# Performance work log

Measured on AMD Instinct MI355X. Metric: run time of the kernel, lower is better.

The kernel has to match this reference:

```python
import jax, jax.numpy as jnp
import numpy as np

PS = 14            # patch size
EMBED = 1024       # vision embed dim
LLM = 2048         # llm embed dim
DS = 2             # downsample factor
B = 8
GRID = 64          # H = W = 64 patches per image
MAX_POS = 4096
ROPE_THETA = 10000.0


def _rope_cache(dim, max_pos, base):
    inv_freq = 1.0 / (base ** (jnp.arange(0, dim, 2, dtype=jnp.float32) / dim))
    t = jnp.arange(max_pos, dtype=jnp.float32)
    freqs = jnp.outer(t, inv_freq)  # [max_pos, dim//2]
    return jnp.cos(freqs), jnp.sin(freqs)


def setup_inputs() -> dict:
    key = jax.random.key(0)
    ks = jax.random.split(key, 5)
    n_total = B * GRID * GRID
    pixel_values = jax.random.normal(ks[0], (n_total, 3, PS, PS), jnp.float32)
    patch_w = jax.random.normal(ks[1], (EMBED, 3, PS, PS), jnp.float32) * (1.0 / np.sqrt(3 * PS * PS))
    patch_b = jax.random.normal(ks[2], (EMBED,), jnp.float32) * 0.02
    dense_w = jax.random.normal(ks[3], (LLM, EMBED, DS, DS), jnp.float32) * (1.0 / np.sqrt(EMBED * DS * DS))
    dense_b = jax.random.normal(ks[4], (LLM,), jnp.float32) * 0.02
    rope_dim = EMBED // 2
    cos_x, sin_x = _rope_cache(rope_dim, MAX_POS, ROPE_THETA)
    cos_y, sin_y = _rope_cache(rope_dim, MAX_POS, ROPE_THETA)
    grid_hw = jnp.full((B, 2), GRID, dtype=jnp.int32)
    return {"pixel_values": pixel_values, "grid_hw": grid_hw,
            "patch_w": patch_w, "patch_b": patch_b,
            "dense_w": dense_w, "dense_b": dense_b,
            "cos_x": cos_x, "sin_x": sin_x, "cos_y": cos_y, "sin_y": sin_y}


def _apply_rotary_1d(x, cos_c, sin_c, pos):
    # x: [N, d], cos_c/sin_c: [max_pos, d//2], pos: [N] int
    c = cos_c[pos]  # gather: [N, d//2]
    s = sin_c[pos]
    x1 = x[:, 0::2]
    x2 = x[:, 1::2]
    o1 = x1 * c - x2 * s
    o2 = x1 * s + x2 * c
    return jnp.stack([o1, o2], axis=-1).reshape(x.shape)  # re-interleave


def _positions(grid_np):
    # grid metadata is static host-side data; build per-patch (x, y) coords
    xs, ys = [], []
    for h, w in grid_np:
        pid = np.arange(h * w)
        xs.append(pid % w)
        ys.append(pid // w)
    return jnp.asarray(np.concatenate(xs)), jnp.asarray(np.concatenate(ys))


def reference(pixel_values, grid_hw, patch_w, patch_b, dense_w, dense_b,
              cos_x, sin_x, cos_y, sin_y):
    grid_np = np.asarray(grid_hw)
    # patchify conv (kernel == stride == patch) is a per-patch linear proj
    pe = jnp.einsum('nchw,echw->ne', pixel_values, patch_w) + patch_b  # [N, E]
    pe = jax.nn.gelu(pe, approximate=False)
    abs_x, abs_y = _positions(grid_np)
    half = EMBED // 2
    p1 = _apply_rotary_1d(pe[:, :half], cos_x, sin_x, abs_x)
    p2 = _apply_rotary_1d(pe[:, half:], cos_y, sin_y, abs_y)
    pe = jnp.concatenate([p1, p2], axis=-1)  # [N, E]
    # per-image downsample conv (kernel == stride == DS): 2x2 block linear
    outs = []
    cur = 0
    for h, w in grid_np:
        x = pe[cur:cur + h * w].reshape(h // DS, DS, w // DS, DS, EMBED)
        o = jnp.einsum('hpwqe,oepq->hwo', x, dense_w) + dense_b
        outs.append(o.reshape(-1, LLM))
        cur += h * w
    return jnp.concatenate(outs, axis=0)
```

## Files before the change

kernel.cpp:

```cpp
#include <hip/hip_runtime.h>
#include <cstdint>


using f16x8 = __attribute__((ext_vector_type(8))) _Float16;
using f32x4 = __attribute__((ext_vector_type(4))) float;

__device__ __forceinline__ void gload_lds16(const void* g, void* l) {
  __builtin_amdgcn_global_load_lds(
      reinterpret_cast<const __attribute__((address_space(1))) unsigned int*>(
          reinterpret_cast<uintptr_t>(g)),
      reinterpret_cast<__attribute__((address_space(3))) unsigned int*>(
          reinterpret_cast<uintptr_t>(l)),
      16, 0, 0);
}

#define BAR   asm volatile("s_barrier" ::: "memory")
#define LGKM0 asm volatile("s_waitcnt lgkmcnt(0)" ::: "memory")
#define VM0   asm volatile("s_waitcnt vmcnt(0)" ::: "memory")

#define KP 640


__global__ void conv_w_kernel(const float* __restrict__ w1,
                              const float* __restrict__ w2,
                              const float* __restrict__ pix,
                              _Float16* __restrict__ h1,
                              _Float16* __restrict__ h2,
                              _Float16* __restrict__ pf) {
  const int bid = blockIdx.x;
  if (bid < 2560) {
    int i = bid * 256 + threadIdx.x;
    int e = i / KP;
    int k = i - e * KP;
    float v = (k < 588) ? w1[(size_t)e * 588 + k] : 0.0f;
    h1[i] = (_Float16)v;
  } else if (bid < 2560 + 8192) {
    int j = (bid - 2560) * 256 + threadIdx.x;
    int o = j >> 10;
    int e = j & 1023;
    const float4 v = *(const float4*)(w2 + (size_t)o * 4096 + e * 4);
    h2[(size_t)o * 4096 + e]        = (_Float16)v.x;
    h2[(size_t)o * 4096 + 1024 + e] = (_Float16)v.y;
    h2[(size_t)o * 4096 + 2048 + e] = (_Float16)v.z;
    h2[(size_t)o * 4096 + 3072 + e] = (_Float16)v.w;
  } else {
    int j = (bid - 2560 - 8192) * 256 + threadIdx.x;
    int n = j / (KP / 8);
    int g = j - n * (KP / 8);
    int k0 = g * 8;
    f16x8 v;
    if (k0 + 8 <= 588) {
      const float4 x0 = *(const float4*)(pix + (size_t)n * 588 + k0);
      const float4 x1 = *(const float4*)(pix + (size_t)n * 588 + k0 + 4);
      v[0] = (_Float16)x0.x; v[1] = (_Float16)x0.y;
      v[2] = (_Float16)x0.z; v[3] = (_Float16)x0.w;
      v[4] = (_Float16)x1.x; v[5] = (_Float16)x1.y;
      v[6] = (_Float16)x1.z; v[7] = (_Float16)x1.w;
    } else {
#pragma unroll
      for (int t = 0; t < 8; ++t) {
        int k = k0 + t;
        v[t] = (k < 588) ? (_Float16)pix[(size_t)n * 588 + k] : (_Float16)0.0f;
      }
    }
    *(f16x8*)(pf + (size_t)n * KP + k0) = v;
  }
}


#define MFMA16(I0, J0, AV, BV)                                                \
  _Pragma("unroll") for (int i_ = 0; i_ < 4; ++i_)                            \
  _Pragma("unroll") for (int j_ = 0; j_ < 2; ++j_)                            \
  _Pragma("unroll") for (int k_ = 0; k_ < 2; ++k_)                            \
      acc[(I0) + i_][(J0) + j_] = __builtin_amdgcn_mfma_f32_16x16x32_f16(     \
          AV[i_][k_], BV[j_][k_], acc[(I0) + i_][(J0) + j_], 0, 0, 0);

#define TILE_BODY(sb)                                                         \
  {                                                                           \
    f16x8 a0[4][2], a1[4][2], vb0[2][2], vb1[2][2];                           \
    _Pragma("unroll") for (int i = 0; i < 4; ++i) {                           \
      a0[i][0] = *(const f16x8*)(lbase + (sb) + aoff + i * 2048 + so0);       \
      a0[i][1] = *(const f16x8*)(lbase + (sb) + aoff + i * 2048 + so1);       \
    }                                                                         \
    _Pragma("unroll") for (int j = 0; j < 2; ++j) {                           \
      vb0[j][0] = *(const f16x8*)(lbase + (sb) + boff + j * 2048 + so0);      \
      vb0[j][1] = *(const f16x8*)(lbase + (sb) + boff + j * 2048 + so1);      \
    }                                                                         \
    MFMA16(0, 0, a0, vb0);                                                    \
    _Pragma("unroll") for (int j = 0; j < 2; ++j) {                           \
      vb1[j][0] = *(const f16x8*)(lbase + (sb) + boff + (2+j) * 2048 + so0);  \
      vb1[j][1] = *(const f16x8*)(lbase + (sb) + boff + (2+j) * 2048 + so1);  \
    }                                                                         \
    MFMA16(0, 2, a0, vb1);                                                    \
    _Pragma("unroll") for (int i = 0; i < 4; ++i) {                           \
      a1[i][0] = *(const f16x8*)(lbase + (sb) + aoff + (4+i) * 2048 + so0);   \
      a1[i][1] = *(const f16x8*)(lbase + (sb) + aoff + (4+i) * 2048 + so1);   \
    }                                                                         \
    MFMA16(4, 2, a1, vb1);                                                    \
    MFMA16(4, 0, a1, vb0);                                                    \
  }


__global__ __launch_bounds__(512, 2) void patch_gemm15(
    const _Float16* __restrict__ pixf,
    const _Float16* __restrict__ b1w,
    const float* __restrict__ bias1,
    const float* __restrict__ cosx, const float* __restrict__ sinx,
    const float* __restrict__ cosy, const float* __restrict__ siny,
    _Float16* __restrict__ peM)
{
  __shared__ _Float16 lds[2][256][64];

  const int tid  = threadIdx.x;
  const int lane = tid & 63;
  const int wave = tid >> 6;
  const int wm = wave >> 2, wn = wave & 3;
  const int bm = blockIdx.x, bn = blockIdx.y;
  const int l15 = lane & 15;
  const int g   = lane >> 4;
  const int s7  = l15 & 7;

  const char* lbase = (const char*)lds;
  char*       lw    = (char*)lds;
  const unsigned aoff = (unsigned)(wm * 16384 + l15 * 128);
  const unsigned boff = (unsigned)(32768 + wn * 8192 + l15 * 128);
  const unsigned so0  = (unsigned)(((0 + g) ^ s7) * 16);
  const unsigned so1  = (unsigned)(((4 + g) ^ s7) * 16);

  const int bm256 = bm * 256, bn256 = bn * 256;
  const int srow = wave * 32 + (lane >> 3);

  auto STAGE = [&](int s) {
    const int c0 = s * 64;
#pragma unroll
    for (int u = 0; u < 4; ++u) {
      const int row  = srow + u * 8;
      const int gcol = (lane & 7) ^ (row & 7);
      gload_lds16(pixf + (size_t)(bm256 + row) * KP + c0 + gcol * 8,
                  lw + (wave * 4 + u) * 1024);
      gload_lds16(b1w + (size_t)(bn256 + row) * KP + c0 + gcol * 8,
                  lw + 32768 + (wave * 4 + u) * 1024);
    }
  };

  f32x4 acc[8][4] = {};

  for (int s = 0; s < 10; ++s) {
    STAGE(s);
    VM0; BAR;
    __builtin_amdgcn_s_setprio(1);
    TILE_BODY(0u);
    __builtin_amdgcn_s_setprio(0);
    LGKM0; BAR;
  }

  BAR;
  float* sw = (float*)(lw) + wave * (16 * 65);
  const int md = (lane >> 4) * 4;
  const int rq = lane & 3;
  const int lr = lane >> 2;
#pragma unroll
  for (int p = 0; p < 8; ++p) {
#pragma unroll
    for (int r = 0; r < 4; ++r) {
      const int lrow = md + r;
#pragma unroll
      for (int nf = 0; nf < 4; ++nf)
        sw[lrow * 65 + nf * 16 + l15] = acc[p][nf][r];
    }
    {
      const int m   = bm256 + wm * 128 + p * 16 + lr;
      const int pid = m & 4095;
      const int yy = pid >> 6, xx = pid & 63;
      const int t  = (m >> 12) * 1024 + (yy >> 1) * 32 + (xx >> 1);
      const int pq = (yy & 1) * 2 + (xx & 1);
      const int e0 = bn256 + wn * 64 + rq * 16;
      const int h2 = (e0 >= 512) ? 1 : 0;
      const int idx0 = (h2 ? (e0 - 512) : e0) >> 1;
      const int pos  = h2 ? yy : xx;
      const float* ct = (h2 ? cosy : cosx) + pos * 256 + idx0;
      const float* st = (h2 ? siny : sinx) + pos * 256 + idx0;
      const float4 c0 = *(const float4*)ct, c1 = *(const float4*)(ct + 4);
      const float4 s0 = *(const float4*)st, s1 = *(const float4*)(st + 4);
      const float4 b0 = *(const float4*)(bias1 + e0);
      const float4 b1 = *(const float4*)(bias1 + e0 + 4);
      const float4 b2 = *(const float4*)(bias1 + e0 + 8);
      const float4 b3 = *(const float4*)(bias1 + e0 + 12);
      const float bb[16] = {b0.x,b0.y,b0.z,b0.w, b1.x,b1.y,b1.z,b1.w,
                            b2.x,b2.y,b2.z,b2.w, b3.x,b3.y,b3.z,b3.w};
      float v[16];
#pragma unroll
      for (int j = 0; j < 16; ++j) {
        float x = sw[lr * 65 + rq * 16 + j] + bb[j];
        v[j] = 0.5f * x * (1.0f + erff(x * 0.70710678118654752f));
      }
      const float cc[8] = {c0.x,c0.y,c0.z,c0.w, c1.x,c1.y,c1.z,c1.w};
      const float ss[8] = {s0.x,s0.y,s0.z,s0.w, s1.x,s1.y,s1.z,s1.w};
      _Float16 o[16];
#pragma unroll
      for (int k = 0; k < 8; ++k) {
        o[2*k]   = (_Float16)(v[2*k] * cc[k] - v[2*k+1] * ss[k]);
        o[2*k+1] = (_Float16)(v[2*k] * ss[k] + v[2*k+1] * cc[k]);
      }
      _Float16* dst = peM + (size_t)t * 4096 + pq * 1024 + e0;
      *(f16x8*)dst       = *(const f16x8*)&o[0];
      *(f16x8*)(dst + 8) = *(const f16x8*)&o[8];
    }
  }
}


__global__ __launch_bounds__(512, 2) void dense_gemm9(
    const _Float16* __restrict__ aM,
    const _Float16* __restrict__ bM,
    const float* __restrict__ bias2, float* __restrict__ out)
{
  __shared__ _Float16 lds[2][2][256][64];

  const int tid  = threadIdx.x;
  const int lane = tid & 63;
  const int wave = tid >> 6;
  const int wm = wave >> 2, wn = wave & 3;
  const int bm = blockIdx.x, bn = blockIdx.y;
  const int l15 = lane & 15;
  const int g   = lane >> 4;
  const int s7  = l15 & 7;

  const char* lbase = (const char*)lds;
  char*       lw    = (char*)lds;
  const unsigned aoff = (unsigned)(wm * 16384 + l15 * 128);
  const unsigned boff = (unsigned)(32768 + wn * 8192 + l15 * 128);
  const unsigned so0  = (unsigned)(((0 + g) ^ s7) * 16);
  const unsigned so1  = (unsigned)(((4 + g) ^ s7) * 16);

  const int bm256 = bm * 256, bn256 = bn * 256;
  const int srow = (wave * 4) * 8 + (lane >> 3);

  auto STAGE = [&](int s) {
    char* slot = lw + ((size_t)(s & 1) << 16);
    const int c0 = s * 64;
#pragma unroll
    for (int u = 0; u < 4; ++u) {
      const int row  = srow + u * 8;
      const int gcol = (lane & 7) ^ (row & 7);
      gload_lds16(aM + (size_t)(bm256 + row) * 4096 + c0 + gcol * 8,
                  slot + (wave * 4 + u) * 1024);
      gload_lds16(bM + (size_t)(bn256 + row) * 4096 + c0 + gcol * 8,
                  slot + 32768 + (wave * 4 + u) * 1024);
    }
  };

  f32x4 acc[8][4] = {};

  STAGE(0); VM0; BAR;
#pragma unroll 2
  for (int s = 0; s < 64; ++s) {
    if (s + 1 < 64) STAGE(s + 1);
    const unsigned sb = (unsigned)((s & 1) << 16);
    __builtin_amdgcn_s_setprio(1);
    TILE_BODY(sb);
    __builtin_amdgcn_s_setprio(0);
    LGKM0; VM0; BAR;
  }

  const int md = (lane >> 4) * 4;
  const int r0 = bm256 + wm * 128;
  const int c0 = bn256 + wn * 64;
#pragma unroll
  for (int nf = 0; nf < 4; ++nf) {
    const int o = c0 + nf * 16 + l15;
    const float bs = bias2[o];
#pragma unroll
    for (int mf = 0; mf < 8; ++mf) {
      const int t_ = r0 + mf * 16 + md;
#pragma unroll
      for (int r = 0; r < 4; ++r)
        out[(size_t)(t_ + r) * 2048 + o] = acc[mf][nf][r] + bs;
    }
  }
}


extern "C" void kernel_launch(void* const* d_in, const int* in_sizes, int n_in,
                              void* d_out, int out_size, void* d_ws, size_t ws_size,
                              hipStream_t stream) {
  const float* pix  = (const float*)d_in[0];
  const float* w1   = (const float*)d_in[2];
  const float* b1   = (const float*)d_in[3];
  const float* w2   = (const float*)d_in[4];
  const float* b2   = (const float*)d_in[5];
  const float* cosx = (const float*)d_in[6];
  const float* sinx = (const float*)d_in[7];
  const float* cosy = (const float*)d_in[8];
  const float* siny = (const float*)d_in[9];
  float* out = (float*)d_out;

  _Float16* ws = (_Float16*)d_ws;
  const size_t PE_N  = (size_t)8192 * 4096;
  const size_t B1_N  = (size_t)1024 * KP;
  const size_t B2_N  = (size_t)2048 * 4096;
  _Float16* peM  = ws;
  _Float16* b1h  = peM + PE_N;
  _Float16* b2h  = b1h + B1_N;
  _Float16* pixf = b2h + B2_N;

  const int pix_blocks = (32768 * (KP / 8)) / 256;
  conv_w_kernel<<<dim3(2560 + 8192 + pix_blocks), dim3(256), 0, stream>>>(
      w1, w2, pix, b1h, b2h, pixf);
  patch_gemm15<<<dim3(128, 4), dim3(512), 0, stream>>>(
      pixf, b1h, b1, cosx, sinx, cosy, siny, peM);
  dense_gemm9<<<dim3(32, 8), dim3(512), 0, stream>>>(
      peM, b2h, b2, out);
}
```

Measured before the change: 255.0 us.

## Fuse fp32-to-fp16 pixel conversion into patch GEMM A-tile loading

Drops the separate pass that converted the pixel tensor to padded fp16 in the workspace. The patch GEMM now reads fp32 pixels directly into registers, converts them, and writes them into swizzled LDS. The next stage's A loads are issued before the MFMA body so they overlap compute. This removes a full read-and-write pass over the pixel data, at the cost of more register pressure and reading fp32 pixels once per column block of the GEMM (four times).

```diff
diff --git a/kernel.cpp b/kernel.cpp
--- a/kernel.cpp
+++ b/kernel.cpp
@@ -3,6 +3,7 @@
 
 
 using f16x8 = __attribute__((ext_vector_type(8))) _Float16;
+using f16x4 = __attribute__((ext_vector_type(4))) _Float16;
 using f32x4 = __attribute__((ext_vector_type(4))) float;
 
 __device__ __forceinline__ void gload_lds16(const void* g, void* l) {
@@ -23,10 +24,8 @@
 
 __global__ void conv_w_kernel(const float* __restrict__ w1,
                               const float* __restrict__ w2,
-                              const float* __restrict__ pix,
                               _Float16* __restrict__ h1,
-                              _Float16* __restrict__ h2,
-                              _Float16* __restrict__ pf) {
+                              _Float16* __restrict__ h2) {
   const int bid = blockIdx.x;
   if (bid < 2560) {
     int i = bid * 256 + threadIdx.x;
@@ -34,7 +33,7 @@
     int k = i - e * KP;
     float v = (k < 588) ? w1[(size_t)e * 588 + k] : 0.0f;
     h1[i] = (_Float16)v;
-  } else if (bid < 2560 + 8192) {
+  } else {
     int j = (bid - 2560) * 256 + threadIdx.x;
     int o = j >> 10;
     int e = j & 1023;
@@ -43,27 +42,6 @@
     h2[(size_t)o * 4096 + 1024 + e] = (_Float16)v.y;
     h2[(size_t)o * 4096 + 2048 + e] = (_Float16)v.z;
     h2[(size_t)o * 4096 + 3072 + e] = (_Float16)v.w;
-  } else {
-    int j = (bid - 2560 - 8192) * 256 + threadIdx.x;
-    int n = j / (KP / 8);
-    int g = j - n * (KP / 8);
-    int k0 = g * 8;
-    f16x8 v;
-    if (k0 + 8 <= 588) {
-      const float4 x0 = *(const float4*)(pix + (size_t)n * 588 + k0);
-      const float4 x1 = *(const float4*)(pix + (size_t)n * 588 + k0 + 4);
-      v[0] = (_Float16)x0.x; v[1] = (_Float16)x0.y;
-      v[2] = (_Float16)x0.z; v[3] = (_Float16)x0.w;
-      v[4] = (_Float16)x1.x; v[5] = (_Float16)x1.y;
-      v[6] = (_Float16)x1.z; v[7] = (_Float16)x1.w;
-    } else {
-#pragma unroll
-      for (int t = 0; t < 8; ++t) {
-        int k = k0 + t;
-        v[t] = (k < 588) ? (_Float16)pix[(size_t)n * 588 + k] : (_Float16)0.0f;
-      }
-    }
-    *(f16x8*)(pf + (size_t)n * KP + k0) = v;
   }
 }
 
@@ -101,8 +79,8 @@
   }
 
 
-__global__ __launch_bounds__(512, 2) void patch_gemm15(
-    const _Float16* __restrict__ pixf,
+__global__ __launch_bounds__(512, 2) void patch_gemm17(
+    const float* __restrict__ pix,
     const _Float16* __restrict__ b1w,
     const float* __restrict__ bias1,
     const float* __restrict__ cosx, const float* __restrict__ sinx,
@@ -129,32 +107,58 @@
 
   const int bm256 = bm * 256, bn256 = bn * 256;
   const int srow = wave * 32 + (lane >> 3);
-
-  auto STAGE = [&](int s) {
+  const int acol = lane & 15;
+  const int arw  = wave * 32 + (lane >> 4);
+
+  auto LOADA = [&](int s, float4 (&ar)[8]) {
+    const bool full = (s < 9);
+#pragma unroll
+    for (int u = 0; u < 8; ++u) {
+      const int row = arw + u * 4;
+      const float* p = pix + (size_t)(bm256 + row) * 588 + s * 64 + acol * 4;
+      if (full || acol < 3) ar[u] = *(const float4*)p;
+      else ar[u] = make_float4(0.f, 0.f, 0.f, 0.f);
+    }
+  };
+  auto WRITEA = [&](float4 (&ar)[8]) {
+    const int c   = acol >> 1;
+    const int sub = acol & 1;
+#pragma unroll
+    for (int u = 0; u < 8; ++u) {
+      const int row = arw + u * 4;
+      f16x4 v;
+      v[0] = (_Float16)ar[u].x; v[1] = (_Float16)ar[u].y;
+      v[2] = (_Float16)ar[u].z; v[3] = (_Float16)ar[u].w;
+      *(f16x4*)(lw + row * 128 + ((c ^ (row & 7)) * 16 + sub * 8)) = v;
+    }
+  };
+  auto STAGE_B = [&](int s) {
     const int c0 = s * 64;
 #pragma unroll
     for (int u = 0; u < 4; ++u) {
       const int row  = srow + u * 8;
       const int gcol = (lane & 7) ^ (row & 7);
-      gload_lds16(pixf + (size_t)(bm256 + row) * KP + c0 + gcol * 8,
-                  lw + (wave * 4 + u) * 1024);
       gload_lds16(b1w + (size_t)(bn256 + row) * KP + c0 + gcol * 8,
                   lw + 32768 + (wave * 4 + u) * 1024);
     }
   };
 
   f32x4 acc[8][4] = {};
-
+  float4 areg[8];
+
+  LOADA(0, areg);
   for (int s = 0; s < 10; ++s) {
-    STAGE(s);
-    VM0; BAR;
+    WRITEA(areg);
+    STAGE_B(s);
+    VM0;
+    LGKM0; BAR;
+    if (s + 1 < 10) LOADA(s + 1, areg);
     __builtin_amdgcn_s_setprio(1);
     TILE_BODY(0u);
     __builtin_amdgcn_s_setprio(0);
     LGKM0; BAR;
   }
 
-  BAR;
   float* sw = (float*)(lw) + wave * (16 * 65);
   const int md = (lane >> 4) * 4;
   const int rq = lane & 3;
@@ -298,17 +302,13 @@
   _Float16* ws = (_Float16*)d_ws;
   const size_t PE_N  = (size_t)8192 * 4096;
   const size_t B1_N  = (size_t)1024 * KP;
-  const size_t B2_N  = (size_t)2048 * 4096;
   _Float16* peM  = ws;
   _Float16* b1h  = peM + PE_N;
   _Float16* b2h  = b1h + B1_N;
-  _Float16* pixf = b2h + B2_N;
-
-  const int pix_blocks = (32768 * (KP / 8)) / 256;
-  conv_w_kernel<<<dim3(2560 + 8192 + pix_blocks), dim3(256), 0, stream>>>(
-      w1, w2, pix, b1h, b2h, pixf);
-  patch_gemm15<<<dim3(128, 4), dim3(512), 0, stream>>>(
-      pixf, b1h, b1, cosx, sinx, cosy, siny, peM);
+
+  conv_w_kernel<<<dim3(2560 + 8192), dim3(256), 0, stream>>>(w1, w2, b1h, b2h);
+  patch_gemm17<<<dim3(128, 4), dim3(512), 0, stream>>>(
+      pix, b1h, b1, cosx, sinx, cosy, siny, peM);
   dense_gemm9<<<dim3(32, 8), dim3(512), 0, stream>>>(
       peM, b2h, b2, out);
 }
```

Result: no change. 251.3 us (-1.4%).
